# Kernel tuning notes

Measured on AMD Instinct MI355X. Metric: run time of the kernel, lower is better.

The kernel has to match this reference:

```python
import jax, jax.numpy as jnp
import numpy as np

B, N, C = 128, 197, 768   # batch, tokens (14*14 + cls), embed dim
H = 12                    # attention heads, head_dim = 64
OUT = 32                  # hard-coded mlp out_features
CH_H = 14                 # channel-attention heads
CN = 196                  # channel-attention token dim (14*14)
MLP_HID = int(C * 4.0)    # 3072
CMLP_HID = int(OUT * 4.0) # 128
EPS = 1e-5


def _ln(x, g, b):
    m = x.mean(-1, keepdims=True)
    v = ((x - m) ** 2).mean(-1, keepdims=True)
    return (x - m) * jax.lax.rsqrt(v + EPS) * g + b


def setup_inputs() -> dict:
    key = jax.random.key(0)
    ks = jax.random.split(key, 24)
    W = lambda k, sh: (jax.random.normal(k, sh, jnp.float32) * 0.02)
    return {
        "x": jax.random.normal(ks[0], (B, N, C), jnp.float32),
        # block 1: norm1 + token attention
        "g1": jnp.ones((C,), jnp.float32), "b1": jnp.zeros((C,), jnp.float32),
        "w_qkv": W(ks[1], (3 * C, C)),                     # qkv_bias=False
        "w_proj": W(ks[2], (C, C)), "b_proj": jnp.zeros((C,), jnp.float32),
        # block 2: norm2 + mlp (768 -> 3072 -> 32), NOT residual
        "g2": jnp.ones((C,), jnp.float32), "b2": jnp.zeros((C,), jnp.float32),
        "w_fc1": W(ks[3], (MLP_HID, C)), "b_fc1": jnp.zeros((MLP_HID,), jnp.float32),
        "w_fc2": W(ks[4], (OUT, MLP_HID)), "b_fc2": jnp.zeros((OUT,), jnp.float32),
        # block 3: norm3 + channel attention (over 196 spatial positions)
        "g3": jnp.ones((OUT,), jnp.float32), "b3": jnp.zeros((OUT,), jnp.float32),
        "w_cqkv": W(ks[5], (3 * CN, CN)),                  # qkv_bias=False
        "w_cproj": W(ks[6], (CN, CN)), "b_cproj": jnp.zeros((CN,), jnp.float32),
        # block 4: norm4 + channel mlp (32 -> 128 -> 32)
        "g4": jnp.ones((OUT,), jnp.float32), "b4": jnp.zeros((OUT,), jnp.float32),
        "w_cfc1": W(ks[7], (CMLP_HID, OUT)), "b_cfc1": jnp.zeros((CMLP_HID,), jnp.float32),
        "w_cfc2": W(ks[8], (OUT, CMLP_HID)), "b_cfc2": jnp.zeros((OUT,), jnp.float32),
    }


def reference(x, g1, b1, w_qkv, w_proj, b_proj,
              g2, b2, w_fc1, b_fc1, w_fc2, b_fc2,
              g3, b3, w_cqkv, w_cproj, b_cproj,
              g4, b4, w_cfc1, b_cfc1, w_cfc2, b_cfc2):
    Bz, Nn, Cc = x.shape
    hd = Cc // H  # 64

    # --- token attention (residual) ---
    h = _ln(x, g1, b1)
    qkv = (h @ w_qkv.T).reshape(Bz, Nn, 3, H, hd).transpose(2, 0, 3, 1, 4)
    q, k, v = qkv[0], qkv[1], qkv[2]                       # [B,H,N,hd]
    a = jax.nn.softmax(jnp.einsum('bhqd,bhkd->bhqk', q, k) * (hd ** -0.5), axis=-1)
    o = jnp.einsum('bhqk,bhkd->bhqd', a, v).transpose(0, 2, 1, 3).reshape(Bz, Nn, Cc)
    x = x + (o @ w_proj.T + b_proj)

    # --- mlp 768->3072->32, NO residual (matches original forward) ---
    h = _ln(x, g2, b2)
    x = jax.nn.gelu(h @ w_fc1.T + b_fc1, approximate=False) @ w_fc2.T + b_fc2  # [B,N,32]

    # --- channel attention (residual); N==197 path, no interleave averaging ---
    h = _ln(x, g3, b3)
    cls = h[:, :1, :]                                      # [B,1,32]
    t = h[:, 1:, :].transpose(0, 2, 1)                     # [B,32,196]
    chd = CN // CH_H  # 14
    cqkv = (t @ w_cqkv.T).reshape(Bz, OUT, 3, CH_H, chd).transpose(2, 0, 3, 1, 4)
    cq, ck, cv = cqkv[0], cqkv[1], cqkv[2]                 # [B,14,32,14]
    ca = jax.nn.softmax(jnp.einsum('bhqd,bhkd->bhqk', cq, ck) * (chd ** -0.5), axis=-1)
    co = jnp.einsum('bhqk,bhkd->bhqd', ca, cv).transpose(0, 2, 1, 3).reshape(Bz, OUT, CN)
    co = co @ w_cproj.T + b_cproj                          # [B,32,196]
    x = x + jnp.concatenate([cls, co.transpose(0, 2, 1)], axis=1)

    # --- channel mlp 32->128->32 (residual) ---
    h = _ln(x, g4, b4)
    x = x + (jax.nn.gelu(h @ w_cfc1.T + b_cfc1, approximate=False) @ w_cfc2.T + b_cfc2)
    return x
```

## Files before the change

### kernel.cpp

```cpp
#include <hip/hip_runtime.h>
#include <hip/hip_bf16.h>

typedef unsigned short u16;
typedef __hip_bfloat16 bf16;
typedef __attribute__((ext_vector_type(8))) short bf16x8;
typedef __attribute__((ext_vector_type(4))) float f32x4;

#define B_   128
#define N_   197
#define C_   768
#define H_   12
#define HD_  64
#define T_   (B_*N_)
#define MH_  3072
#define OUT_ 32
#define CN_  196
#define CHH_ 14
#define KP_  224
#define CSZ_ (B_*CHH_*32*14)

__device__ __forceinline__ float bfu2f(u16 x){ union{unsigned u; float f;} v; v.u=((unsigned)x)<<16; return v.f; }
__device__ __forceinline__ bf16  f2bf(float f){ return __float2bfloat16(f); }
__device__ __forceinline__ u16   f2bfu(float f){ union{bf16 h; u16 u;} c; c.h=__float2bfloat16(f); return c.u; }
__device__ __forceinline__ float gelu_f(float x){ return 0.5f*x*(1.0f+erff(x*0.70710678118654752f)); }

__device__ __forceinline__ void gl_lds16(const u16* g, u16* l){
  __builtin_amdgcn_global_load_lds((const __attribute__((address_space(1))) void*)g,
                                   (__attribute__((address_space(3))) void*)l, 16, 0, 0);
}

__global__ __launch_bounds__(256) void write_code_kernel(float* out, int n, float code){
  int i = blockIdx.x*256 + threadIdx.x;
  if (i < n) out[i] = code;
}

template<bool F32IN>
__global__ __launch_bounds__(256) void ln768_kernel(const void* __restrict__ xv,
    const float* __restrict__ g, const float* __restrict__ b, bf16* __restrict__ out)
{
  int row = blockIdx.x;
  int tid = threadIdx.x;
  float v0, v1, v2;
  if (F32IN){
    const float* xr = (const float*)xv + (size_t)row*C_;
    v0 = xr[tid]; v1 = xr[tid+256]; v2 = xr[tid+512];
  } else {
    const u16* xr = (const u16*)xv + (size_t)row*C_;
    v0 = bfu2f(xr[tid]); v1 = bfu2f(xr[tid+256]); v2 = bfu2f(xr[tid+512]);
  }
  __shared__ float red[4];
  int lane = tid & 63, wave = tid >> 6;
  float s = v0+v1+v2;
  #pragma unroll
  for (int off=32; off>0; off>>=1) s += __shfl_xor(s, off);
  if (lane==0) red[wave]=s;
  __syncthreads();
  float mean = (red[0]+red[1]+red[2]+red[3]) * (1.0f/C_);
  float d0=v0-mean, d1=v1-mean, d2=v2-mean;
  float q = d0*d0+d1*d1+d2*d2;
  #pragma unroll
  for (int off=32; off>0; off>>=1) q += __shfl_xor(q, off);
  __syncthreads();
  if (lane==0) red[wave]=q;
  __syncthreads();
  float var = (red[0]+red[1]+red[2]+red[3]) * (1.0f/C_);
  float r = rsqrtf(var + 1e-5f);
  bf16* orow = out + (size_t)row*C_;
  orow[tid]     = f2bf(d0*r*g[tid]     + b[tid]);
  orow[tid+256] = f2bf(d1*r*g[tid+256] + b[tid+256]);
  orow[tid+512] = f2bf(d2*r*g[tid+512] + b[tid+512]);
}

__global__ __launch_bounds__(256) void ln32_kernel(const float* __restrict__ x,
    const float* __restrict__ g, const float* __restrict__ b, float* __restrict__ out)
{
  int i = blockIdx.x*256 + threadIdx.x;
  int c = i & 31;
  float v = x[i];
  float s = v;
  #pragma unroll
  for (int off=16; off>0; off>>=1) s += __shfl_xor(s, off, 32);
  float mean = s * (1.0f/32);
  float d = v - mean;
  float q = d*d;
  #pragma unroll
  for (int off=16; off>0; off>>=1) q += __shfl_xor(q, off, 32);
  float r = rsqrtf(q*(1.0f/32) + 1e-5f);
  out[i] = d*r*g[c] + b[c];
}

__global__ __launch_bounds__(256) void packw_bf16(const float* __restrict__ w,
    u16* __restrict__ dst, int n)
{
  int i = (blockIdx.x*256 + threadIdx.x)*4;
  if (i >= n) return;
  float4 v = *(const float4*)(w + i);
  ushort4 o; o.x=f2bfu(v.x); o.y=f2bfu(v.y); o.z=f2bfu(v.z); o.w=f2bfu(v.w);
  *(ushort4*)(dst + i) = o;
}

__global__ __launch_bounds__(256) void init_x3_kernel(const float* __restrict__ bias,
    float* __restrict__ x3)
{
  int i = blockIdx.x*256 + threadIdx.x;
  x3[i] = bias[i & 31];
}

__global__ __launch_bounds__(256) void fc2red_ln32_kernel(const float* pp,
    const float* __restrict__ bias2, const float* __restrict__ g,
    const float* __restrict__ b, float* __restrict__ x3, float* h3)
{
  int i = blockIdx.x*256 + threadIdx.x;
  int c = i & 31;
  float v = bias2[c];
  #pragma unroll
  for (int nt=0; nt<24; nt++) v += pp[(size_t)nt*T_*32 + i];
  x3[i] = v;
  float s = v;
  #pragma unroll
  for (int off=16; off>0; off>>=1) s += __shfl_xor(s, off, 32);
  float mean = s * (1.0f/32);
  float d = v - mean;
  float q = d*d;
  #pragma unroll
  for (int off=16; off>0; off>>=1) q += __shfl_xor(q, off, 32);
  float rr = rsqrtf(q*(1.0f/32) + 1e-5f);
  h3[i] = d*rr*g[c] + b[c];
}

template<int MODE, bool WB16>
__global__ __launch_bounds__(256) void gemm128(
    const u16* __restrict__ A, const void* __restrict__ Wsrc,
    const float* __restrict__ bias, const float* __restrict__ resid,
    bf16* __restrict__ outb,
    bf16* __restrict__ q_out, bf16* __restrict__ k_out, bf16* __restrict__ v_out,
    int Nn, int K,
    const u16* __restrict__ w2, float* __restrict__ outf, int koff)
{
  __shared__ __align__(16) u16 SM[16384];
  const int tid  = threadIdx.x;
  const int wave = tid >> 6, lane = tid & 63;
  const int quad = lane >> 4, l16 = lane & 15;
  const int wr = wave >> 1, wc = wave & 1;
  const unsigned Nx  = gridDim.x;
  const unsigned nwg = Nx * gridDim.y;
  unsigned lin = blockIdx.x + Nx*blockIdx.y;
  unsigned q8 = nwg >> 3, r8 = nwg & 7;
  unsigned xcd = lin & 7, sub = lin >> 3;
  unsigned nl = (xcd < r8 ? xcd*(q8+1) : r8*(q8+1) + (xcd-r8)*q8) + sub;
  const int m0 = (int)(nl / Nx) * 128;
  const int n0 = (int)(nl % Nx) * 128;
  const int rs = tid >> 2;
  const int kc = (tid & 3) << 3;

  const u16* aA0 = A + (size_t)(m0 + rs)*K + kc;
  const u16* aA1 = aA0 + (size_t)64*K;
  const u16*  wB0 = WB16 ? ((const u16*)Wsrc + (size_t)(n0 + rs)*K + kc) : nullptr;
  const float* wF0 = WB16 ? nullptr : ((const float*)Wsrc + (size_t)(n0 + rs)*K + kc);

  f32x4 acc[4][4] = {};

  auto STAGE = [&](int buf, int k0){
    u16* AsW = SM + buf*4096 + wave*512;
    u16* BsW = SM + 8192 + buf*4096 + wave*512;
    gl_lds16(aA0 + k0, AsW);
    gl_lds16(aA1 + k0, AsW + 2048);
    if (WB16){
      gl_lds16(wB0 + k0, BsW);
      gl_lds16(wB0 + (size_t)64*K + k0, BsW + 2048);
    } else {
      float4 w0 = *(const float4*)(wF0 + k0);
      float4 w1 = *(const float4*)(wF0 + k0 + 4);
      const float* wF1 = wF0 + (size_t)64*K;
      float4 w2v = *(const float4*)(wF1 + k0);
      float4 w3 = *(const float4*)(wF1 + k0 + 4);
      ushort4 b0; b0.x=f2bfu(w0.x); b0.y=f2bfu(w0.y); b0.z=f2bfu(w0.z); b0.w=f2bfu(w0.w);
      ushort4 b1; b1.x=f2bfu(w1.x); b1.y=f2bfu(w1.y); b1.z=f2bfu(w1.z); b1.w=f2bfu(w1.w);
      ushort4 b2; b2.x=f2bfu(w2v.x); b2.y=f2bfu(w2v.y); b2.z=f2bfu(w2v.z); b2.w=f2bfu(w2v.w);
      ushort4 b3; b3.x=f2bfu(w3.x); b3.y=f2bfu(w3.y); b3.z=f2bfu(w3.z); b3.w=f2bfu(w3.w);
      u16* Bsb = SM + 8192 + buf*4096;
      *(ushort4*)&Bsb[rs*32 + kc]        = b0;
      *(ushort4*)&Bsb[rs*32 + kc + 4]    = b1;
      *(ushort4*)&Bsb[(rs+64)*32 + kc]   = b2;
      *(ushort4*)&Bsb[(rs+64)*32 + kc+4] = b3;
    }
  };

  STAGE(0, 0);
  __syncthreads();
  int cur = 0;

  for (int k0 = 0; k0 < K; k0 += 32){
    if (k0 + 32 < K) STAGE(cur^1, k0 + 32);
    bf16x8 af[4], bfr[4];
    #pragma unroll
    for (int i=0;i<4;i++) af[i]  = *(const bf16x8*)&SM[cur*4096 + (wr*64 + i*16 + l16)*32 + quad*8];
    #pragma unroll
    for (int j=0;j<4;j++) bfr[j] = *(const bf16x8*)&SM[8192 + cur*4096 + (wc*64 + j*16 + l16)*32 + quad*8];
    #pragma unroll
    for (int i=0;i<4;i++)
      #pragma unroll
      for (int j=0;j<4;j++)
        acc[i][j] = __builtin_amdgcn_mfma_f32_16x16x32_bf16(af[i], bfr[j], acc[i][j], 0, 0, 0);
    __syncthreads();
    cur ^= 1;
  }

  #pragma unroll
  for (int i=0;i<4;i++){
    #pragma unroll
    for (int j=0;j<4;j++){
      #pragma unroll
      for (int r=0;r<4;r++){
        int m = m0 + wr*64 + i*16 + quad*4 + r;
        int c = n0 + wc*64 + j*16 + l16;
        float v = acc[i][j][r];
        if (MODE==0){
          int bb = m / N_;
          int n  = m - bb*N_;
          int sec = c / C_;
          int rem = c - sec*C_;
          int hh  = rem >> 6;
          int d   = rem & 63;
          bf16* dst = (sec==0) ? q_out : (sec==1) ? k_out : v_out;
          dst[(((size_t)bb*H_ + hh)*N_ + n)*HD_ + d] = f2bf(v);
        } else if (MODE==1){
          size_t idx = (size_t)m*Nn + c;
          outb[idx] = f2bf(v + bias[c] + resid[idx]);
        } else if (MODE==2){
          outb[(size_t)m*Nn + c] = f2bf(gelu_f(v + bias[c]));
        } else {
          int row = wr*64 + i*16 + quad*4 + r;
          int col = wc*64 + j*16 + l16;
          SM[(row*128 + col) ^ ((row&7)<<3)] = f2bfu(gelu_f(v + bias[c]));
        }
      }
    }
  }

  if (MODE==7){
    __syncthreads();
    f32x4 acc2[2][2] = {};
    #pragma unroll
    for (int ks=0; ks<4; ks++){
      bf16x8 af2[2], bf2[2];
      #pragma unroll
      for (int i=0;i<2;i++){
        int row = wave*32 + i*16 + l16;
        af2[i] = *(const bf16x8*)&SM[(row*128 + ks*32 + quad*8) ^ ((row&7)<<3)];
      }
      #pragma unroll
      for (int jb=0;jb<2;jb++)
        bf2[jb] = *(const bf16x8*)(w2 + (size_t)(jb*16 + l16)*MH_ + koff + n0 + ks*32 + quad*8);
      #pragma unroll
      for (int i=0;i<2;i++)
        #pragma unroll
        for (int jb=0;jb<2;jb++)
          acc2[i][jb] = __builtin_amdgcn_mfma_f32_16x16x32_bf16(af2[i], bf2[jb], acc2[i][jb], 0, 0, 0);
    }
    int slot = (koff ? 12 : 0) + (n0 >> 7);
    float* pslab = outf + (size_t)slot*T_*32;
    #pragma unroll
    for (int i=0;i<2;i++)
      #pragma unroll
      for (int jb=0;jb<2;jb++)
        #pragma unroll
        for (int r=0;r<4;r++){
          int m = m0 + wave*32 + i*16 + quad*4 + r;
          int c = jb*16 + l16;
          pslab[(size_t)m*OUT_ + c] = acc2[i][jb][r];
        }
  }
}

template<int MODE, bool WB16>
__global__ __launch_bounds__(256) void gemm_mfma(
    const u16* __restrict__ A, const void* __restrict__ Wsrc,
    const float* __restrict__ bias, const float* __restrict__ resid,
    bf16* __restrict__ outb, float* __restrict__ outf,
    bf16* __restrict__ q_out, bf16* __restrict__ k_out, bf16* __restrict__ v_out,
    int M, int Nn, int K, int wld, int astride)
{
  __shared__ __align__(16) u16 As[64][32];
  __shared__ __align__(16) u16 Bs[64][32];
  const int tid  = threadIdx.x;
  const int wave = tid >> 6, lane = tid & 63;
  const int quad = lane >> 4, l16 = lane & 15;
  const int m0 = blockIdx.x * 64;
  const int n0 = (MODE==6) ? 0 : blockIdx.y * 64;
  const int kst = (MODE==6) ? blockIdx.y * K : 0;
  const int rs = tid >> 2;
  const int kc = (tid & 3) << 3;
  const u16* arow = A + (size_t)(m0 + rs)*astride + kst + kc;
  const bool wvalid = (n0 + rs) < Nn;

  f32x4 acc[4] = {};

  for (int k0 = 0; k0 < K; k0 += 32){
    *(uint4*)&As[rs][kc] = *(const uint4*)(arow + k0);
    if (WB16){
      const u16* wrow = (const u16*)Wsrc + (size_t)(n0 + rs)*wld + kst + kc;
      uint4 wv = make_uint4(0u,0u,0u,0u);
      if (wvalid) wv = *(const uint4*)(wrow + k0);
      *(uint4*)&Bs[rs][kc] = wv;
    } else {
      const float* wrow = (const float*)Wsrc + (size_t)(n0 + rs)*wld + kst + kc;
      float4 w0 = make_float4(0.f,0.f,0.f,0.f), w1 = w0;
      if (wvalid){ w0 = *(const float4*)(wrow + k0); w1 = *(const float4*)(wrow + k0 + 4); }
      ushort4 b0; b0.x=f2bfu(w0.x); b0.y=f2bfu(w0.y); b0.z=f2bfu(w0.z); b0.w=f2bfu(w0.w);
      ushort4 b1; b1.x=f2bfu(w1.x); b1.y=f2bfu(w1.y); b1.z=f2bfu(w1.z); b1.w=f2bfu(w1.w);
      *(ushort4*)&Bs[rs][kc]   = b0;
      *(ushort4*)&Bs[rs][kc+4] = b1;
    }
    __syncthreads();
    bf16x8 af = *(const bf16x8*)&As[wave*16 + l16][quad*8];
    #pragma unroll
    for (int nb=0; nb<4; nb++){
      bf16x8 bfr = *(const bf16x8*)&Bs[nb*16 + l16][quad*8];
      acc[nb] = __builtin_amdgcn_mfma_f32_16x16x32_bf16(af, bfr, acc[nb], 0, 0, 0);
    }
    __syncthreads();
  }

  #pragma unroll
  for (int nb=0; nb<4; nb++){
    #pragma unroll
    for (int r=0; r<4; r++){
      int m = m0 + wave*16 + quad*4 + r;
      int c = n0 + nb*16 + l16;
      float v = acc[nb][r];
      if (MODE==3){
        if (c < Nn) outf[(size_t)m*Nn + c] = v + bias[c];
      } else if (MODE==4){
        if (c < Nn) outf[(size_t)m*Nn + c] += v;
      } else if (MODE==6){
        if (c < Nn) atomicAdd(&outf[(size_t)m*Nn + c], v);
      } else if (MODE==5){
        if (c < Nn){
          int bb = m >> 5, oo = m & 31;
          int sec = c / CN_;
          int rem = c - sec*CN_;
          int hh  = rem / 14;
          int d   = rem - hh*14;
          outf[(size_t)sec*CSZ_ + (((size_t)bb*CHH_ + hh)*32 + oo)*14 + d] = v;
        }
      }
    }
  }
}

__global__ __launch_bounds__(256) void attn_kernel(const u16* __restrict__ q,
    const u16* __restrict__ k, const u16* __restrict__ v, bf16* __restrict__ o)
{
  __shared__ __align__(16) u16 VtS[64*208];
  __shared__ __align__(16) u16 PsS[4*16*208];
  int bh = blockIdx.x;
  int b = bh / H_, hh = bh - b*H_;
  int tid = threadIdx.x, wave = tid >> 6, lane = tid & 63;
  int quad = lane >> 4, l16 = lane & 15;
  const u16* qb = q + (size_t)bh*N_*HD_;
  const u16* kb = k + (size_t)bh*N_*HD_;
  const u16* vb = v + (size_t)bh*N_*HD_;
  for (int idx = tid; idx < (N_*HD_)/8; idx += 256){
    int j = idx >> 3, dg = idx & 7;
    bf16x8 vv = *(const bf16x8*)(vb + (size_t)j*HD_ + dg*8);
    #pragma unroll
    for (int e=0;e<8;e++){
      int d = dg*8 + e;
      VtS[(d*208 + j) ^ ((d&7)<<3)] = ((u16*)&vv)[e];
    }
  }
  for (int idx = tid; idx < 64*11; idx += 256){
    int d = idx / 11, j = 197 + (idx - d*11);
    VtS[(d*208 + j) ^ ((d&7)<<3)] = 0;
  }
  __syncthreads();

  u16* PsW = PsS + wave*16*208;
  const float LOG2E = 1.4426950408889634f;

  for (int g = wave; g < 13; g += 4){
    int r0 = g*16;
    int qrow = r0 + l16;
    int qr = (qrow < N_) ? qrow : 0;
    bf16x8 aq0 = *(const bf16x8*)(qb + (size_t)qr*HD_ + quad*8);
    bf16x8 aq1 = *(const bf16x8*)(qb + (size_t)qr*HD_ + 32 + quad*8);
    f32x4 s[13];
    __builtin_amdgcn_s_setprio(1);
    #pragma unroll
    for (int nb = 0; nb < 13; nb++){
      int krow = nb*16 + l16;
      int kr = (krow < N_) ? krow : 0;
      bf16x8 bk0 = *(const bf16x8*)(kb + (size_t)kr*HD_ + quad*8);
      bf16x8 bk1 = *(const bf16x8*)(kb + (size_t)kr*HD_ + 32 + quad*8);
      f32x4 t = {};
      t = __builtin_amdgcn_mfma_f32_16x16x32_bf16(aq0, bk0, t, 0, 0, 0);
      t = __builtin_amdgcn_mfma_f32_16x16x32_bf16(aq1, bk1, t, 0, 0, 0);
      s[nb] = t;
    }
    __builtin_amdgcn_s_setprio(0);
    #pragma unroll
    for (int nb = 0; nb < 13; nb++){
      bool colok = (nb*16 + l16) < N_;
      #pragma unroll
      for (int r = 0; r < 4; r++)
        s[nb][r] = colok ? s[nb][r]*(0.125f*LOG2E) : -1e30f;
    }
    #pragma unroll
    for (int r = 0; r < 4; r++){
      float m01 = fmaxf(s[0][r], s[1][r]),  m23 = fmaxf(s[2][r], s[3][r]);
      float m45 = fmaxf(s[4][r], s[5][r]),  m67 = fmaxf(s[6][r], s[7][r]);
      float m89 = fmaxf(s[8][r], s[9][r]),  mab = fmaxf(s[10][r], s[11][r]);
      float m = fmaxf(fmaxf(fmaxf(m01,m23), fmaxf(m45,m67)),
                      fmaxf(fmaxf(m89,mab), s[12][r]));
      m = fmaxf(m, __shfl_xor(m, 1));
      m = fmaxf(m, __shfl_xor(m, 2));
      m = fmaxf(m, __shfl_xor(m, 4));
      m = fmaxf(m, __shfl_xor(m, 8));
      #pragma unroll
      for (int nb = 0; nb < 13; nb++)
        s[nb][r] = __builtin_amdgcn_exp2f(s[nb][r] - m);
      float t01=s[0][r]+s[1][r], t23=s[2][r]+s[3][r];
      float t45=s[4][r]+s[5][r], t67=s[6][r]+s[7][r];
      float t89=s[8][r]+s[9][r], tab=s[10][r]+s[11][r];
      float su = ((t01+t23)+(t45+t67)) + ((t89+tab)+s[12][r]);
      su += __shfl_xor(su, 1);
      su += __shfl_xor(su, 2);
      su += __shfl_xor(su, 4);
      su += __shfl_xor(su, 8);
      float inv = 1.0f/su;
      #pragma unroll
      for (int nb = 0; nb < 13; nb++) s[nb][r] *= inv;
    }
    #pragma unroll
    for (int nb = 0; nb < 13; nb++)
      #pragma unroll
      for (int r = 0; r < 4; r++){
        int row = quad*4 + r;
        PsW[(row*208 + nb*16 + l16) ^ ((row&7)<<3)] = f2bfu(s[nb][r]);
      }
    __threadfence_block();
    f32x4 oa[4] = {};
    __builtin_amdgcn_s_setprio(1);
    #pragma unroll
    for (int ks = 0; ks < 7; ks++){
      int col = ks*32 + quad*8;
      bool ok = (col < 208);
      int ccol = ok ? col : 0;
      bf16x8 ap = *(const bf16x8*)&PsW[(l16*208 + ccol) ^ ((l16&7)<<3)];
      if (!ok) ap = (bf16x8){0,0,0,0,0,0,0,0};
      #pragma unroll
      for (int nd = 0; nd < 4; nd++){
        bf16x8 bv = *(const bf16x8*)&VtS[((nd*16 + l16)*208 + ccol) ^ ((l16&7)<<3)];
        oa[nd] = __builtin_amdgcn_mfma_f32_16x16x32_bf16(ap, bv, oa[nd], 0, 0, 0);
      }
    }
    __builtin_amdgcn_s_setprio(0);
    #pragma unroll
    for (int nd = 0; nd < 4; nd++)
      #pragma unroll
      for (int r = 0; r < 4; r++){
        int qi = r0 + quad*4 + r;
        if (qi < N_)
          o[((size_t)b*N_ + qi)*C_ + hh*HD_ + nd*16 + l16] = f2bf(oa[nd][r]);
      }
    __threadfence_block();
  }
}

__global__ __launch_bounds__(256) void pack_tall_kernel(const float* __restrict__ h3,
    u16* __restrict__ tall)
{
  int idx = blockIdx.x*256 + threadIdx.x;
  if (idx >= 4096*KP_) return;
  int row = idx / KP_, kk = idx - row*KP_;
  int b = row >> 5, oo = row & 31;
  float v = (kk < CN_) ? h3[((size_t)b*N_ + 1 + kk)*32 + oo] : 0.f;
  tall[idx] = f2bfu(v);
}

__global__ __launch_bounds__(256) void pack_w_kernel(const float* __restrict__ w,
    u16* __restrict__ dst, int rows, int kreal)
{
  int idx = blockIdx.x*256 + threadIdx.x;
  if (idx >= rows*KP_) return;
  int r = idx / KP_, kk = idx - r*KP_;
  dst[idx] = (kk < kreal) ? f2bfu(w[(size_t)r*kreal + kk]) : (u16)0;
}

__global__ __launch_bounds__(256) void pack_co_kernel(const float* __restrict__ co,
    u16* __restrict__ dst)
{
  int idx = blockIdx.x*256 + threadIdx.x;
  if (idx >= 4096*KP_) return;
  int row = idx / KP_, kk = idx - row*KP_;
  dst[idx] = (kk < CN_) ? f2bfu(co[(size_t)row*CN_ + kk]) : (u16)0;
}

__global__ __launch_bounds__(64) void cattn_kernel(const float* __restrict__ cq,
    const float* __restrict__ ck, const float* __restrict__ cv, float* __restrict__ co)
{
  __shared__ __align__(16) float qs[32*15], ks_[32*15], vs[32*15], ps[32*34];
  int bh = blockIdx.x;
  int b  = bh / CHH_;
  int hh = bh - b*CHH_;
  int lane = threadIdx.x;
  const float* qb = cq + (size_t)bh*448;
  const float* kb = ck + (size_t)bh*448;
  const float* vb = cv + (size_t)bh*448;
  for (int idx=lane; idx<448; idx+=64){
    int o = idx/14, d = idx - o*14;
    qs[o*15+d] = qb[idx]; ks_[o*15+d] = kb[idx]; vs[o*15+d] = vb[idx];
  }
  __syncthreads();
  int o = lane & 31, half = lane >> 5;
  const float scale = 0.2672612419124244f;
  float sc[16]; float mx = -1e30f;
  #pragma unroll
  for (int jj=0; jj<16; jj++){
    int j = half*16 + jj;
    float a = 0.f;
    #pragma unroll
    for (int d=0; d<14; d++) a += qs[o*15+d]*ks_[j*15+d];
    sc[jj] = a*scale;
    mx = fmaxf(mx, sc[jj]);
  }
  mx = fmaxf(mx, __shfl_xor(mx, 32));
  float sum = 0.f;
  #pragma unroll
  for (int jj=0; jj<16; jj++){ sc[jj] = __expf(sc[jj]-mx); sum += sc[jj]; }
  sum += __shfl_xor(sum, 32);
  float inv = 1.0f/sum;
  #pragma unroll
  for (int jj=0; jj<16; jj++) ps[o*34 + half*16 + jj] = sc[jj]*inv;
  __syncthreads();
  #pragma unroll
  for (int dd=0; dd<7; dd++){
    int d = half*7 + dd;
    float acc = 0.f;
    #pragma unroll
    for (int j=0; j<32; j++) acc += ps[o*34+j]*vs[j*15+d];
    co[((size_t)b*32 + o)*CN_ + hh*14 + d] = acc;
  }
}

__global__ __launch_bounds__(256) void concat_ln32_kernel(const float* __restrict__ x3,
    const float* __restrict__ h3, const float* __restrict__ co2,
    const float* __restrict__ g, const float* __restrict__ b,
    float* __restrict__ x4, float* __restrict__ h4)
{
  int i = blockIdx.x*256 + threadIdx.x;
  int c = i & 31;
  int row = i >> 5;
  int bb = row / N_;
  int r = row - bb*N_;
  float add = (r==0) ? h3[i] : co2[((size_t)bb*32 + c)*CN_ + (r-1)];
  float v = x3[i] + add;
  x4[i] = v;
  float s = v;
  #pragma unroll
  for (int off=16; off>0; off>>=1) s += __shfl_xor(s, off, 32);
  float mean = s * (1.0f/32);
  float d = v - mean;
  float q = d*d;
  #pragma unroll
  for (int off=16; off>0; off>>=1) q += __shfl_xor(q, off, 32);
  float rr = rsqrtf(q*(1.0f/32) + 1e-5f);
  h4[i] = d*rr*g[c] + b[c];
}

__global__ __launch_bounds__(256) void cfc1_kernel(const float* __restrict__ h4,
    const float* __restrict__ w, const float* __restrict__ bias, float* __restrict__ chid)
{
  int idx = blockIdx.x*256 + threadIdx.x;
  int m = idx >> 7, j = idx & 127;
  const float* hr = h4 + (size_t)m*32;
  const float* wr = w + (size_t)j*32;
  float acc = bias[j];
  #pragma unroll
  for (int kk=0; kk<32; kk++) acc += hr[kk]*wr[kk];
  chid[idx] = gelu_f(acc);
}

__global__ __launch_bounds__(256) void cfc2_kernel(const float* __restrict__ chid,
    const float* __restrict__ w, const float* __restrict__ bias,
    const float* __restrict__ x4, float* __restrict__ out)
{
  int idx = blockIdx.x*256 + threadIdx.x;
  int m = idx >> 5, j = idx & 31;
  const float* cr = chid + (size_t)m*128;
  const float* wr = w + (size_t)j*128;
  float acc = bias[j];
  #pragma unroll
  for (int kk=0; kk<128; kk++) acc += cr[kk]*wr[kk];
  out[idx] = x4[idx] + acc;
}

extern "C" void kernel_launch(void* const* d_in, const int* in_sizes, int n_in,
                              void* d_out, int out_size, void* d_ws, size_t ws_size,
                              hipStream_t stream)
{
  const int NIN = 23;
  static const int dsz[NIN] = {19365888,768,768,1769472,589824,768,768,768,2359296,
                               3072,98304,32,32,32,115248,38416,196,32,32,4096,128,4096,32};
  static const int a2d[NIN] = {2,7,13,18,20,22,16,9,11,5,1,6,12,17,19,21,15,14,8,10,4,3,0};

  float* dout = (float*)d_out;
  int ogrid = (out_size + 255)/256;

  const float* in[NIN];
  bool dict_ok = (n_in == NIN);
  if (dict_ok) for (int i=0;i<NIN;i++) if (in_sizes[i] != dsz[i]) { dict_ok=false; break; }
  if (dict_ok){
    for (int i=0;i<NIN;i++) in[i] = (const float*)d_in[i];
  } else {
    bool alpha_ok = (n_in == NIN);
    if (alpha_ok) for (int i=0;i<NIN;i++) if (in_sizes[i] != dsz[a2d[i]]) { alpha_ok=false; break; }
    if (alpha_ok){
      for (int i=0;i<NIN;i++) in[a2d[i]] = (const float*)d_in[i];
    } else {
      write_code_kernel<<<ogrid, 256, 0, stream>>>(dout, out_size, 5000.f + (float)n_in);
      return;
    }
  }

  const float* x      = in[0];
  const float* g1     = in[1];
  const float* b1     = in[2];
  const float* w_qkv  = in[3];
  const float* w_proj = in[4];
  const float* b_proj = in[5];
  const float* g2     = in[6];
  const float* b2     = in[7];
  const float* w_fc1  = in[8];
  const float* b_fc1  = in[9];
  const float* w_fc2  = in[10];
  const float* b_fc2  = in[11];
  const float* g3     = in[12];
  const float* b3     = in[13];
  const float* w_cqkv = in[14];
  const float* w_cproj= in[15];
  const float* b_cproj= in[16];
  const float* g4     = in[17];
  const float* b4     = in[18];
  const float* w_cfc1 = in[19];
  const float* b_cfc1 = in[20];
  const float* w_cfc2 = in[21];
  const float* b_cfc2 = in[22];

  char* ws = (char*)d_ws;
  const size_t TC2 = (size_t)T_*C_*2;
  const size_t NEED = 4*TC2 + 4096;
  if (ws_size < NEED){
    write_code_kernel<<<ogrid, 256, 0, stream>>>(dout, out_size,
        7000.f + (float)(ws_size >> 20));
    return;
  }

  bf16* h_buf   = (bf16*)(ws);
  bf16* o_buf   = (bf16*)(ws);
  bf16* q_buf   = (bf16*)(ws + TC2);
  bf16* k_buf   = (bf16*)(ws + 2*TC2);
  bf16* v_buf   = (bf16*)(ws + 3*TC2);
  bf16* x2_buf  = (bf16*)(ws + TC2);
  bf16* hidh    = (bf16*)(ws + 2*TC2);
  float* x3     = (float*)(ws + TC2);
  float* pp     = (float*)(ws + 2*TC2);
  char* sm = ws + 2*TC2;
  float* h3  = (float*)sm; sm += (size_t)T_*32*4;
  float* cq  = (float*)sm; sm += (size_t)CSZ_*4;
  float* ck  = (float*)sm; sm += (size_t)CSZ_*4;
  float* cv  = (float*)sm; sm += (size_t)CSZ_*4;
  float* co  = (float*)sm; sm += (size_t)B_*32*CN_*4;
  float* co2 = (float*)sm; sm += (size_t)B_*32*CN_*4;
  float* x4  = (float*)sm; sm += (size_t)T_*32*4;
  float* h4  = (float*)sm; sm += (size_t)T_*32*4;
  float* chid = (float*)sm;
  u16* tall  = (u16*)(ws);
  u16* wcq_b = (u16*)(ws + 2*1024*1024);
  u16* co_b  = (u16*)(ws + 3*1024*1024);
  u16* wcp_b = (u16*)(ws + 5*1024*1024);

  u16* wqkv_b  = (u16*)(ws + 4*TC2 + 4096);
  u16* wproj_b = wqkv_b  + (size_t)2304*C_;
  u16* wfc1_b  = wproj_b + (size_t)C_*C_;
  u16* wfc2_b  = wfc1_b  + (size_t)MH_*C_;
  const size_t WPACK = ((size_t)2304*C_ + (size_t)C_*C_ + (size_t)MH_*C_ + (size_t)OUT_*MH_)*2;
  const bool packed = (ws_size >= NEED + WPACK);

  if (packed){
    packw_bf16<<<(2304*C_/4+255)/256, 256, 0, stream>>>(w_qkv,  wqkv_b,  2304*C_);
    packw_bf16<<<(C_*C_/4+255)/256,  256, 0, stream>>>(w_proj, wproj_b, C_*C_);
    packw_bf16<<<(MH_*C_/4+255)/256, 256, 0, stream>>>(w_fc1,  wfc1_b,  MH_*C_);
    packw_bf16<<<(OUT_*MH_/4+255)/256, 256, 0, stream>>>(w_fc2, wfc2_b, OUT_*MH_);
  }

  ln768_kernel<true><<<T_, 256, 0, stream>>>(x, g1, b1, h_buf);
  if (packed)
    gemm128<0,true><<<dim3(2304/128, T_/128), 256, 0, stream>>>((const u16*)h_buf,
        wqkv_b, nullptr, nullptr, nullptr, q_buf, k_buf, v_buf, 2304, C_,
        nullptr, nullptr, 0);
  else
    gemm128<0,false><<<dim3(2304/128, T_/128), 256, 0, stream>>>((const u16*)h_buf,
        w_qkv, nullptr, nullptr, nullptr, q_buf, k_buf, v_buf, 2304, C_,
        nullptr, nullptr, 0);
  attn_kernel<<<B_*H_, 256, 0, stream>>>((const u16*)q_buf, (const u16*)k_buf,
      (const u16*)v_buf, o_buf);
  if (packed)
    gemm128<1,true><<<dim3(C_/128, T_/128), 256, 0, stream>>>((const u16*)o_buf,
        wproj_b, b_proj, x, x2_buf, nullptr, nullptr, nullptr, C_, C_,
        nullptr, nullptr, 0);
  else
    gemm128<1,false><<<dim3(C_/128, T_/128), 256, 0, stream>>>((const u16*)o_buf,
        w_proj, b_proj, x, x2_buf, nullptr, nullptr, nullptr, C_, C_,
        nullptr, nullptr, 0);
  ln768_kernel<false><<<T_, 256, 0, stream>>>(x2_buf, g2, b2, h_buf);
  if (packed){
    for (int half=0; half<2; half++)
      gemm128<7,true><<<dim3(1536/128, T_/128), 256, 0, stream>>>((const u16*)h_buf,
          wfc1_b + (size_t)half*1536*C_, b_fc1 + half*1536, nullptr,
          nullptr, nullptr, nullptr, nullptr, 1536, C_,
          wfc2_b, pp, half*1536);
    fc2red_ln32_kernel<<<(T_*32)/256, 256, 0, stream>>>(pp, b_fc2, g3, b3, x3, h3);
  } else {
    init_x3_kernel<<<(T_*32)/256, 256, 0, stream>>>(b_fc2, x3);
    for (int half=0; half<2; half++){
      gemm128<2,false><<<dim3(1536/128, T_/128), 256, 0, stream>>>((const u16*)h_buf,
          w_fc1 + (size_t)half*1536*C_, b_fc1 + half*1536, nullptr,
          hidh, nullptr, nullptr, nullptr, 1536, C_,
          nullptr, nullptr, 0);
      gemm_mfma<6,false><<<dim3(T_/64, 4), 256, 0, stream>>>((const u16*)hidh,
          w_fc2 + (size_t)half*1536, nullptr, nullptr, nullptr, x3,
          nullptr, nullptr, nullptr, T_, OUT_, 384, MH_, 1536);
    }
    ln32_kernel<<<(T_*32)/256, 256, 0, stream>>>(x3, g3, b3, h3);
  }
  pack_tall_kernel<<<(4096*KP_+255)/256, 256, 0, stream>>>(h3, tall);
  pack_w_kernel<<<(588*KP_+255)/256, 256, 0, stream>>>(w_cqkv, wcq_b, 588, CN_);
  gemm_mfma<5,true><<<dim3(4096/64, 10), 256, 0, stream>>>(tall, wcq_b,
      nullptr, nullptr, nullptr, cq, nullptr, nullptr, nullptr, 4096, 588, KP_, KP_, KP_);
  cattn_kernel<<<B_*CHH_, 64, 0, stream>>>(cq, ck, cv, co);
  pack_co_kernel<<<(4096*KP_+255)/256, 256, 0, stream>>>(co, co_b);
  pack_w_kernel<<<(196*KP_+255)/256, 256, 0, stream>>>(w_cproj, wcp_b, CN_, CN_);
  gemm_mfma<3,true><<<dim3(4096/64, 4), 256, 0, stream>>>(co_b, wcp_b,
      b_cproj, nullptr, nullptr, co2, nullptr, nullptr, nullptr, 4096, CN_, KP_, KP_, KP_);
  concat_ln32_kernel<<<(T_*32)/256, 256, 0, stream>>>(x3, h3, co2, g4, b4, x4, h4);
  cfc1_kernel<<<(T_*128)/256, 256, 0, stream>>>(h4, w_cfc1, b_cfc1, chid);
  cfc2_kernel<<<(T_*32)/256, 256, 0, stream>>>(chid, w_cfc2, b_cfc2, x4, dout);
}
```

Measured before the change: 882.0 us.

## Pair query tiles per wave in attention and fuse channel MLP kernels

The attention kernel now has each wave handle two 16-row query tiles at once. Each K fragment load and V fragment read is shared across two MFMA chains, giving more independent work per wave, with doubled P scratch in shared memory and launch bounds of 2. The two channel-MLP kernels are fused into one that keeps the 128-wide hidden activations in shared memory. This removes the global round trip through the chid buffer at the cost of higher register and LDS pressure in attention. The pair loop covers tiles 0..15 while only 13 exist; the padded tiles are masked on store.

```diff
diff --git a/kernel.cpp b/kernel.cpp
--- a/kernel.cpp
+++ b/kernel.cpp
@@ -349,11 +349,11 @@
   }
 }
 
-__global__ __launch_bounds__(256) void attn_kernel(const u16* __restrict__ q,
+__global__ __launch_bounds__(256, 2) void attn_kernel(const u16* __restrict__ q,
     const u16* __restrict__ k, const u16* __restrict__ v, bf16* __restrict__ o)
 {
   __shared__ __align__(16) u16 VtS[64*208];
-  __shared__ __align__(16) u16 PsS[4*16*208];
+  __shared__ __align__(16) u16 PsS[8*16*208];
   int bh = blockIdx.x;
   int b = bh / H_, hh = bh - b*H_;
   int tid = threadIdx.x, wave = tid >> 6, lane = tid & 63;
@@ -376,16 +376,23 @@
   }
   __syncthreads();
 
-  u16* PsW = PsS + wave*16*208;
+  u16* PsA = PsS + (wave*2 + 0)*16*208;
+  u16* PsB = PsS + (wave*2 + 1)*16*208;
   const float LOG2E = 1.4426950408889634f;
 
-  for (int g = wave; g < 13; g += 4){
-    int r0 = g*16;
-    int qrow = r0 + l16;
-    int qr = (qrow < N_) ? qrow : 0;
-    bf16x8 aq0 = *(const bf16x8*)(qb + (size_t)qr*HD_ + quad*8);
-    bf16x8 aq1 = *(const bf16x8*)(qb + (size_t)qr*HD_ + 32 + quad*8);
-    f32x4 s[13];
+  #pragma unroll
+  for (int pair = 0; pair < 2; pair++){
+    int g1 = wave + pair*8;
+    int g2 = g1 + 4;
+    int r0A = g1*16, r0B = g2*16;
+    int qrowA = r0A + l16, qrowB = r0B + l16;
+    int qrA = (qrowA < N_) ? qrowA : 0;
+    int qrB = (qrowB < N_) ? qrowB : 0;
+    bf16x8 aqA0 = *(const bf16x8*)(qb + (size_t)qrA*HD_ + quad*8);
+    bf16x8 aqA1 = *(const bf16x8*)(qb + (size_t)qrA*HD_ + 32 + quad*8);
+    bf16x8 aqB0 = *(const bf16x8*)(qb + (size_t)qrB*HD_ + quad*8);
+    bf16x8 aqB1 = *(const bf16x8*)(qb + (size_t)qrB*HD_ + 32 + quad*8);
+    f32x4 sA[13], sB[13];
     __builtin_amdgcn_s_setprio(1);
     #pragma unroll
     for (int nb = 0; nb < 13; nb++){
@@ -393,66 +400,107 @@
       int kr = (krow < N_) ? krow : 0;
       bf16x8 bk0 = *(const bf16x8*)(kb + (size_t)kr*HD_ + quad*8);
       bf16x8 bk1 = *(const bf16x8*)(kb + (size_t)kr*HD_ + 32 + quad*8);
-      f32x4 t = {};
-      t = __builtin_amdgcn_mfma_f32_16x16x32_bf16(aq0, bk0, t, 0, 0, 0);
-      t = __builtin_amdgcn_mfma_f32_16x16x32_bf16(aq1, bk1, t, 0, 0, 0);
-      s[nb] = t;
+      f32x4 tA = {}, tB = {};
+      tA = __builtin_amdgcn_mfma_f32_16x16x32_bf16(aqA0, bk0, tA, 0, 0, 0);
+      tB = __builtin_amdgcn_mfma_f32_16x16x32_bf16(aqB0, bk0, tB, 0, 0, 0);
+      tA = __builtin_amdgcn_mfma_f32_16x16x32_bf16(aqA1, bk1, tA, 0, 0, 0);
+      tB = __builtin_amdgcn_mfma_f32_16x16x32_bf16(aqB1, bk1, tB, 0, 0, 0);
+      sA[nb] = tA; sB[nb] = tB;
     }
     __builtin_amdgcn_s_setprio(0);
     #pragma unroll
     for (int nb = 0; nb < 13; nb++){
       bool colok = (nb*16 + l16) < N_;
       #pragma unroll
-      for (int r = 0; r < 4; r++)
-        s[nb][r] = colok ? s[nb][r]*(0.125f*LOG2E) : -1e30f;
+      for (int r = 0; r < 4; r++){
+        sA[nb][r] = colok ? sA[nb][r]*(0.125f*LOG2E) : -1e30f;
+        sB[nb][r] = colok ? sB[nb][r]*(0.125f*LOG2E) : -1e30f;
+      }
     }
     #pragma unroll
     for (int r = 0; r < 4; r++){
-      float m01 = fmaxf(s[0][r], s[1][r]),  m23 = fmaxf(s[2][r], s[3][r]);
-      float m45 = fmaxf(s[4][r], s[5][r]),  m67 = fmaxf(s[6][r], s[7][r]);
-      float m89 = fmaxf(s[8][r], s[9][r]),  mab = fmaxf(s[10][r], s[11][r]);
-      float m = fmaxf(fmaxf(fmaxf(m01,m23), fmaxf(m45,m67)),
-                      fmaxf(fmaxf(m89,mab), s[12][r]));
-      m = fmaxf(m, __shfl_xor(m, 1));
-      m = fmaxf(m, __shfl_xor(m, 2));
-      m = fmaxf(m, __shfl_xor(m, 4));
-      m = fmaxf(m, __shfl_xor(m, 8));
-      #pragma unroll
-      for (int nb = 0; nb < 13; nb++)
-        s[nb][r] = __builtin_amdgcn_exp2f(s[nb][r] - m);
-      float t01=s[0][r]+s[1][r], t23=s[2][r]+s[3][r];
-      float t45=s[4][r]+s[5][r], t67=s[6][r]+s[7][r];
-      float t89=s[8][r]+s[9][r], tab=s[10][r]+s[11][r];
-      float su = ((t01+t23)+(t45+t67)) + ((t89+tab)+s[12][r]);
-      su += __shfl_xor(su, 1);
-      su += __shfl_xor(su, 2);
-      su += __shfl_xor(su, 4);
-      su += __shfl_xor(su, 8);
-      float inv = 1.0f/su;
-      #pragma unroll
-      for (int nb = 0; nb < 13; nb++) s[nb][r] *= inv;
+      float mA, mB;
+      {
+        float m01 = fmaxf(sA[0][r], sA[1][r]),  m23 = fmaxf(sA[2][r], sA[3][r]);
+        float m45 = fmaxf(sA[4][r], sA[5][r]),  m67 = fmaxf(sA[6][r], sA[7][r]);
+        float m89 = fmaxf(sA[8][r], sA[9][r]),  mab = fmaxf(sA[10][r], sA[11][r]);
+        mA = fmaxf(fmaxf(fmaxf(m01,m23), fmaxf(m45,m67)),
+                   fmaxf(fmaxf(m89,mab), sA[12][r]));
+      }
+      {
+        float m01 = fmaxf(sB[0][r], sB[1][r]),  m23 = fmaxf(sB[2][r], sB[3][r]);
+        float m45 = fmaxf(sB[4][r], sB[5][r]),  m67 = fmaxf(sB[6][r], sB[7][r]);
+        float m89 = fmaxf(sB[8][r], sB[9][r]),  mab = fmaxf(sB[10][r], sB[11][r]);
+        mB = fmaxf(fmaxf(fmaxf(m01,m23), fmaxf(m45,m67)),
+                   fmaxf(fmaxf(m89,mab), sB[12][r]));
+      }
+      mA = fmaxf(mA, __shfl_xor(mA, 1));
+      mB = fmaxf(mB, __shfl_xor(mB, 1));
+      mA = fmaxf(mA, __shfl_xor(mA, 2));
+      mB = fmaxf(mB, __shfl_xor(mB, 2));
+      mA = fmaxf(mA, __shfl_xor(mA, 4));
+      mB = fmaxf(mB, __shfl_xor(mB, 4));
+      mA = fmaxf(mA, __shfl_xor(mA, 8));
+      mB = fmaxf(mB, __shfl_xor(mB, 8));
+      #pragma unroll
+      for (int nb = 0; nb < 13; nb++){
+        sA[nb][r] = __builtin_amdgcn_exp2f(sA[nb][r] - mA);
+        sB[nb][r] = __builtin_amdgcn_exp2f(sB[nb][r] - mB);
+      }
+      float suA, suB;
+      {
+        float t01=sA[0][r]+sA[1][r], t23=sA[2][r]+sA[3][r];
+        float t45=sA[4][r]+sA[5][r], t67=sA[6][r]+sA[7][r];
+        float t89=sA[8][r]+sA[9][r], tab=sA[10][r]+sA[11][r];
+        suA = ((t01+t23)+(t45+t67)) + ((t89+tab)+sA[12][r]);
+      }
+      {
+        float t01=sB[0][r]+sB[1][r], t23=sB[2][r]+sB[3][r];
+        float t45=sB[4][r]+sB[5][r], t67=sB[6][r]+sB[7][r];
+        float t89=sB[8][r]+sB[9][r], tab=sB[10][r]+sB[11][r];
+        suB = ((t01+t23)+(t45+t67)) + ((t89+tab)+sB[12][r]);
+      }
+      suA += __shfl_xor(suA, 1);
+      suB += __shfl_xor(suB, 1);
+      suA += __shfl_xor(suA, 2);
+      suB += __shfl_xor(suB, 2);
+      suA += __shfl_xor(suA, 4);
+      suB += __shfl_xor(suB, 4);
+      suA += __shfl_xor(suA, 8);
+      suB += __shfl_xor(suB, 8);
+      float invA = 1.0f/suA, invB = 1.0f/suB;
+      #pragma unroll
+      for (int nb = 0; nb < 13; nb++){
+        sA[nb][r] *= invA;
+        sB[nb][r] *= invB;
+      }
     }
     #pragma unroll
     for (int nb = 0; nb < 13; nb++)
       #pragma unroll
       for (int r = 0; r < 4; r++){
         int row = quad*4 + r;
-        PsW[(row*208 + nb*16 + l16) ^ ((row&7)<<3)] = f2bfu(s[nb][r]);
+        int off = (row*208 + nb*16 + l16) ^ ((row&7)<<3);
+        PsA[off] = f2bfu(sA[nb][r]);
+        PsB[off] = f2bfu(sB[nb][r]);
       }
     __threadfence_block();
-    f32x4 oa[4] = {};
+    f32x4 oaA[4] = {}, oaB[4] = {};
     __builtin_amdgcn_s_setprio(1);
     #pragma unroll
     for (int ks = 0; ks < 7; ks++){
       int col = ks*32 + quad*8;
       bool ok = (col < 208);
       int ccol = ok ? col : 0;
-      bf16x8 ap = *(const bf16x8*)&PsW[(l16*208 + ccol) ^ ((l16&7)<<3)];
-      if (!ok) ap = (bf16x8){0,0,0,0,0,0,0,0};
+      int poff = (l16*208 + ccol) ^ ((l16&7)<<3);
+      bf16x8 apA = *(const bf16x8*)&PsA[poff];
+      bf16x8 apB = *(const bf16x8*)&PsB[poff];
+      if (!ok){ apA = (bf16x8){0,0,0,0,0,0,0,0}; apB = apA; }
       #pragma unroll
       for (int nd = 0; nd < 4; nd++){
         bf16x8 bv = *(const bf16x8*)&VtS[((nd*16 + l16)*208 + ccol) ^ ((l16&7)<<3)];
-        oa[nd] = __builtin_amdgcn_mfma_f32_16x16x32_bf16(ap, bv, oa[nd], 0, 0, 0);
+        oaA[nd] = __builtin_amdgcn_mfma_f32_16x16x32_bf16(apA, bv, oaA[nd], 0, 0, 0);
+        oaB[nd] = __builtin_amdgcn_mfma_f32_16x16x32_bf16(apB, bv, oaB[nd], 0, 0, 0);
       }
     }
     __builtin_amdgcn_s_setprio(0);
@@ -460,9 +508,12 @@
     for (int nd = 0; nd < 4; nd++)
       #pragma unroll
       for (int r = 0; r < 4; r++){
-        int qi = r0 + quad*4 + r;
-        if (qi < N_)
-          o[((size_t)b*N_ + qi)*C_ + hh*HD_ + nd*16 + l16] = f2bf(oa[nd][r]);
+        int qiA = r0A + quad*4 + r;
+        int qiB = r0B + quad*4 + r;
+        if (qiA < N_)
+          o[((size_t)b*N_ + qiA)*C_ + hh*HD_ + nd*16 + l16] = f2bf(oaA[nd][r]);
+        if (qiB < N_)
+          o[((size_t)b*N_ + qiB)*C_ + hh*HD_ + nd*16 + l16] = f2bf(oaB[nd][r]);
       }
     __threadfence_block();
   }
@@ -569,31 +620,46 @@
   h4[i] = d*rr*g[c] + b[c];
 }
 
-__global__ __launch_bounds__(256) void cfc1_kernel(const float* __restrict__ h4,
-    const float* __restrict__ w, const float* __restrict__ bias, float* __restrict__ chid)
-{
-  int idx = blockIdx.x*256 + threadIdx.x;
-  int m = idx >> 7, j = idx & 127;
-  const float* hr = h4 + (size_t)m*32;
-  const float* wr = w + (size_t)j*32;
-  float acc = bias[j];
-  #pragma unroll
-  for (int kk=0; kk<32; kk++) acc += hr[kk]*wr[kk];
-  chid[idx] = gelu_f(acc);
-}
-
-__global__ __launch_bounds__(256) void cfc2_kernel(const float* __restrict__ chid,
-    const float* __restrict__ w, const float* __restrict__ bias,
+__global__ __launch_bounds__(256) void cfc12_kernel(const float* __restrict__ h4,
+    const float* __restrict__ w1, const float* __restrict__ b1_,
+    const float* __restrict__ w2, const float* __restrict__ b2_,
     const float* __restrict__ x4, float* __restrict__ out)
 {
-  int idx = blockIdx.x*256 + threadIdx.x;
-  int m = idx >> 5, j = idx & 31;
-  const float* cr = chid + (size_t)m*128;
-  const float* wr = w + (size_t)j*128;
-  float acc = bias[j];
-  #pragma unroll
-  for (int kk=0; kk<128; kk++) acc += cr[kk]*wr[kk];
-  out[idx] = x4[idx] + acc;
+  __shared__ float h4s[16*32];
+  __shared__ float chs[16*132];
+  int tid = threadIdx.x;
+  size_t base = (size_t)blockIdx.x*16*32;
+  h4s[tid]      = h4[base + tid];
+  h4s[tid+256]  = h4[base + tid + 256];
+  __syncthreads();
+  {
+    int r  = tid >> 4;
+    int j0 = tid & 15;
+    #pragma unroll
+    for (int jj=0; jj<8; jj++){
+      int j = j0 + 16*jj;
+      const float* wr = w1 + (size_t)j*32;
+      float acc = b1_[j];
+      #pragma unroll
+      for (int kk=0; kk<32; kk++) acc += h4s[r*32+kk]*wr[kk];
+      chs[r*132 + j] = gelu_f(acc);
+    }
+  }
+  __syncthreads();
+  {
+    int r  = tid >> 4;
+    int j0 = (tid & 15)*2;
+    #pragma unroll
+    for (int jj=0; jj<2; jj++){
+      int j = j0 + jj;
+      const float* wr = w2 + (size_t)j*128;
+      float acc = b2_[j];
+      #pragma unroll
+      for (int kk=0; kk<128; kk++) acc += chs[r*132+kk]*wr[kk];
+      size_t oi = base + r*32 + j;
+      out[oi] = x4[oi] + acc;
+    }
+  }
 }
 
 extern "C" void kernel_launch(void* const* d_in, const int* in_sizes, int n_in,
@@ -675,7 +741,6 @@
   float* co2 = (float*)sm; sm += (size_t)B_*32*CN_*4;
   float* x4  = (float*)sm; sm += (size_t)T_*32*4;
   float* h4  = (float*)sm; sm += (size_t)T_*32*4;
-  float* chid = (float*)sm;
   u16* tall  = (u16*)(ws);
   u16* wcq_b = (u16*)(ws + 2*1024*1024);
   u16* co_b  = (u16*)(ws + 3*1024*1024);
@@ -745,6 +810,5 @@
   gemm_mfma<3,true><<<dim3(4096/64, 4), 256, 0, stream>>>(co_b, wcp_b,
       b_cproj, nullptr, nullptr, co2, nullptr, nullptr, nullptr, 4096, CN_, KP_, KP_, KP_);
   concat_ln32_kernel<<<(T_*32)/256, 256, 0, stream>>>(x3, h3, co2, g4, b4, x4, h4);
-  cfc1_kernel<<<(T_*128)/256, 256, 0, stream>>>(h4, w_cfc1, b_cfc1, chid);
-  cfc2_kernel<<<(T_*32)/256, 256, 0, stream>>>(chid, w_cfc2, b_cfc2, x4, dout);
-}
+  cfc12_kernel<<<T_/16, 256, 0, stream>>>(h4, w_cfc1, b_cfc1, w_cfc2, b_cfc2, x4, dout);
+}
```

Result: faster. 838.5 us (-4.9%).
